# Optimization experiments

Measured on AMD Instinct MI355X. Metric: run time of the kernel, lower is better.

## Reference

```python
import jax, jax.numpy as jnp
import numpy as np

B, T, C = 2, 2048, 2048
H, KVH, HD = 16, 4, 128  # heads, kv heads, head_dim
G = H // KVH             # GQA group size
THETA = 10000.0


def _rope_cos_sin(t, hd, dtype):
    inv_freq = 1.0 / (THETA ** (jnp.arange(0, hd, 2, dtype=jnp.float32) / hd))
    pos = jnp.arange(t, dtype=jnp.float32)
    freqs = pos[:, None] * inv_freq[None, :]          # [T, hd/2]
    emb = jnp.concatenate([freqs, freqs], axis=-1)    # [T, hd]
    return jnp.cos(emb).astype(dtype), jnp.sin(emb).astype(dtype)


def _rotate_half(x):
    x1, x2 = jnp.split(x, 2, axis=-1)
    return jnp.concatenate([-x2, x1], axis=-1)


def setup_inputs() -> dict:
    key = jax.random.key(0)
    ks = jax.random.split(key, 5)
    s_in = 1.0 / np.sqrt(C)
    return {
        "x": jax.random.normal(ks[0], (B, T, C), jnp.float32),
        "wq": jax.random.normal(ks[1], (C, H * HD), jnp.float32) * s_in,
        "bq": jnp.zeros((H * HD,), jnp.float32),
        "wk": jax.random.normal(ks[2], (C, KVH * HD), jnp.float32) * s_in,
        "bk": jnp.zeros((KVH * HD,), jnp.float32),
        "wv": jax.random.normal(ks[3], (C, KVH * HD), jnp.float32) * s_in,
        "bv": jnp.zeros((KVH * HD,), jnp.float32),
        "wo": jax.random.normal(ks[4], (H * HD, C), jnp.float32) * (1.0 / np.sqrt(H * HD)),
    }


def reference(x, wq, bq, wk, bk, wv, bv, wo):
    b, t, c = x.shape
    q = (x @ wq + bq).reshape(b, t, H, HD).transpose(0, 2, 1, 3)    # [B,H,T,hd]
    k = (x @ wk + bk).reshape(b, t, KVH, HD).transpose(0, 2, 1, 3)  # [B,KVH,T,hd]
    v = (x @ wv + bv).reshape(b, t, KVH, HD).transpose(0, 2, 1, 3)

    cos, sin = _rope_cos_sin(t, HD, x.dtype)  # [T,hd]
    q = q * cos + _rotate_half(q) * sin
    k = k * cos + _rotate_half(k) * sin

    # GQA: group query heads over kv heads
    qg = q.reshape(b, KVH, G, t, HD)
    scale = 1.0 / np.sqrt(HD)
    scores = jnp.einsum('bkgtd,bksd->bkgts', qg, k) * scale  # [B,KVH,G,T,T]
    causal = jnp.tril(jnp.ones((t, t), bool))
    scores = jnp.where(causal, scores, jnp.finfo(scores.dtype).min)
    attn = jax.nn.softmax(scores, axis=-1)
    out = jnp.einsum('bkgts,bksd->bkgtd', attn, v)            # [B,KVH,G,T,hd]
    out = out.reshape(b, H, t, HD).transpose(0, 2, 1, 3).reshape(b, t, H * HD)
    return out @ wo
```

## Files before the change

### kernel.cpp

```cpp
#include <hip/hip_runtime.h>
#include <hip/hip_bf16.h>
#include <math.h>

#define B_ 2
#define T_ 2048
#define C_ 2048
#define H_ 16
#define KVH_ 4
#define HD_ 128
#define G_ (H_ / KVH_)
#define MROWS (B_ * T_)
#define NQKV (H_ * HD_ + 2 * KVH_ * HD_)
#define KOFF (H_ * HD_)
#define VOFF (H_ * HD_ + KVH_ * HD_)

typedef __hip_bfloat16 bf16;
typedef short bf16x8 __attribute__((ext_vector_type(8)));
typedef short bf16x4 __attribute__((ext_vector_type(4)));
typedef float f32x4 __attribute__((ext_vector_type(4)));

__device__ __forceinline__ void gload_lds16(const void* g, void* l) {
  __builtin_amdgcn_global_load_lds(
      (const __attribute__((address_space(1))) unsigned int*)g,
      (__attribute__((address_space(3))) unsigned int*)l, 16, 0, 0);
}

static __device__ __forceinline__ f32x4 mfma16(bf16x4 a, bf16x4 b, f32x4 c) {
#if __has_builtin(__builtin_amdgcn_mfma_f32_16x16x16_bf16)
  return __builtin_amdgcn_mfma_f32_16x16x16_bf16(a, b, c, 0, 0, 0);
#else
  return __builtin_amdgcn_mfma_f32_16x16x16bf16_1k(a, b, c, 0, 0, 0);
#endif
}

static __device__ __forceinline__ short f2bf(float x) {
  unsigned u = __builtin_bit_cast(unsigned, x);
  u += 0x7FFFu + ((u >> 16) & 1u);
  return (short)(u >> 16);
}

static __device__ __forceinline__ float fexp2(float x) {
#if __has_builtin(__builtin_amdgcn_exp2f)
  return __builtin_amdgcn_exp2f(x);
#else
  return exp2f(x);
#endif
}

__global__ void cast_bf16_kernel(const float* __restrict__ in, bf16* __restrict__ out, int n) {
  int i = (blockIdx.x * 256 + threadIdx.x) * 4;
  if (i >= n) return;
  float4 v = *(const float4*)(in + i);
  out[i + 0] = __float2bfloat16(v.x);
  out[i + 1] = __float2bfloat16(v.y);
  out[i + 2] = __float2bfloat16(v.z);
  out[i + 3] = __float2bfloat16(v.w);
}

__global__ __launch_bounds__(256) void transpose_cast(const float* __restrict__ in,
                                                      bf16* __restrict__ out,
                                                      int R, int Ccols) {
  __shared__ float t[32][33];
  const int tx = threadIdx.x & 31, ty = threadIdx.x >> 5;
  const int r0 = blockIdx.y * 32, c0 = blockIdx.x * 32;
#pragma unroll
  for (int it = 0; it < 4; ++it)
    t[ty + 8 * it][tx] = in[(size_t)(r0 + ty + 8 * it) * Ccols + c0 + tx];
  __syncthreads();
#pragma unroll
  for (int it = 0; it < 4; ++it)
    out[(size_t)(c0 + ty + 8 * it) * R + r0 + tx] = __float2bfloat16(t[tx][ty + 8 * it]);
}

__global__ __launch_bounds__(256) void transpose_v(const bf16* __restrict__ qkv,
                                                   bf16* __restrict__ vt) {
  __shared__ bf16 t[32][33];
  const int tx = threadIdx.x & 31, ty = threadIdx.x >> 5;
  const int b = blockIdx.z >> 2, kvh = blockIdx.z & 3;
  const int t0 = blockIdx.x * 32, d0 = blockIdx.y * 32;
#pragma unroll
  for (int it = 0; it < 4; ++it)
    t[ty + 8 * it][tx] =
        qkv[(size_t)(b * T_ + t0 + ty + 8 * it) * NQKV + VOFF + kvh * HD_ + d0 + tx];
  __syncthreads();
#pragma unroll
  for (int it = 0; it < 4; ++it)
    vt[((size_t)((b * KVH_ + kvh) * HD_) + d0 + ty + 8 * it) * T_ + t0 + tx] =
        t[tx][ty + 8 * it];
}

__global__ void rope_bf16(bf16* __restrict__ buf, int ld, int col0, int nheads) {
  const int row = blockIdx.x / nheads;
  const int h = blockIdx.x % nheads;
  const int t = row % T_;
  const int d = threadIdx.x;
  bf16* rp = buf + (size_t)row * ld + col0 + h * HD_;
  float vd = __bfloat162float(rp[d]);
  float vp = __bfloat162float(rp[d ^ 64]);
  __syncthreads();
  const int i = d & 63;
  float invf = expf(-(float)(2 * i) * (9.210340371976184f / 128.0f));
  float ang = (float)t * invf;
  float c = cosf(ang), s = sinf(ang);
  rp[d] = __float2bfloat16((d < 64) ? (vd * c - vp * s) : (vd * c + vp * s));
}

template <bool BF16OUT>
__global__ __launch_bounds__(256, 2) void gemm_mfma(
    const bf16* __restrict__ A, const bf16* __restrict__ Bt, void* __restrict__ Cout,
    const float* __restrict__ bq, const float* __restrict__ bk2,
    const float* __restrict__ bv2, int M, int N, int K) {
  __shared__ __align__(16) bf16 As[128 * 32];
  __shared__ __align__(16) bf16 Bs[128 * 32];
  const int tid = threadIdx.x;
  const int w = tid >> 6, lane = tid & 63;
  const int colL = lane & 15, quad = lane >> 4;
  const int wm = w & 1, wn = w >> 1;
  const int r0 = blockIdx.y * 128, c0 = blockIdx.x * 128;

  f32x4 acc[4][4];
  const f32x4 zero = {0.f, 0.f, 0.f, 0.f};
#pragma unroll
  for (int mt = 0; mt < 4; ++mt)
#pragma unroll
    for (int nt = 0; nt < 4; ++nt) acc[mt][nt] = zero;

  for (int k0 = 0; k0 < K; k0 += 32) {
    __syncthreads();
#pragma unroll
    for (int it = 0; it < 2; ++it) {
      const int seg = it * 4 + w;
      const int idx = seg * 64 + lane;
      const int row = idx >> 2, off = idx & 3;
      gload_lds16(A + (size_t)(r0 + row) * K + k0 + off * 8, &As[seg * 512]);
      gload_lds16(Bt + (size_t)(c0 + row) * K + k0 + off * 8, &Bs[seg * 512]);
    }
    __syncthreads();
    bf16x8 af[4], bfv[4];
#pragma unroll
    for (int mt = 0; mt < 4; ++mt)
      af[mt] = *(const bf16x8*)&As[(wm * 64 + mt * 16 + colL) * 32 + quad * 8];
#pragma unroll
    for (int nt = 0; nt < 4; ++nt)
      bfv[nt] = *(const bf16x8*)&Bs[(wn * 64 + nt * 16 + colL) * 32 + quad * 8];
#pragma unroll
    for (int mt = 0; mt < 4; ++mt)
#pragma unroll
      for (int nt = 0; nt < 4; ++nt)
        acc[mt][nt] =
            __builtin_amdgcn_mfma_f32_16x16x32_bf16(af[mt], bfv[nt], acc[mt][nt], 0, 0, 0);
  }

#pragma unroll
  for (int nt = 0; nt < 4; ++nt) {
    const int c = c0 + wn * 64 + nt * 16 + colL;
    float bias = 0.f;
    if (bq) bias = (c < KOFF) ? bq[c] : (c < VOFF ? bk2[c - KOFF] : bv2[c - VOFF]);
#pragma unroll
    for (int mt = 0; mt < 4; ++mt) {
#pragma unroll
      for (int i = 0; i < 4; ++i) {
        const int r = r0 + wm * 64 + mt * 16 + quad * 4 + i;
        const float v = acc[mt][nt][i] + bias;
        if (BF16OUT)
          ((bf16*)Cout)[(size_t)r * N + c] = __float2bfloat16(v);
        else
          ((float*)Cout)[(size_t)r * N + c] = v;
      }
    }
  }
}

#define FA_SCL2 (0.08838834764831845f * 1.4426950408889634f)
#define FA_M2 16.0f

__global__ __launch_bounds__(256, 2) void flash_mfma4(
    const bf16* __restrict__ qkv, const bf16* __restrict__ vt, bf16* __restrict__ ao) {
  __shared__ __align__(16) char smem[32768];
  bf16* Kb0 = (bf16*)smem;
  bf16* Kb1 = (bf16*)(smem + 8192);
  bf16* Vb0 = (bf16*)(smem + 16384);
  bf16* Vb1 = (bf16*)(smem + 24576);

  const int id = blockIdx.x;
  const int hb = id >> 4;
  const int qq = id & 15;
  const int qt = (hb & 1) ? (15 - qq) : qq;
  const int h = hb & 15, b = hb >> 4;
  const int kvh = h >> 2;
  const int q0 = qt * 128;

  const int tid = threadIdx.x;
  const int w = tid >> 6, lane = tid & 63;
  const int colL = lane & 15, quad = lane >> 4;
  const int myq0 = q0 + w * 32;

  const bf16* kg = qkv + (size_t)(b * T_) * NQKV + KOFF + kvh * HD_;
  const bf16* vg = vt + (size_t)((b * KVH_ + kvh) * HD_) * T_;

  auto stageKV = [&](int tile, bf16* kl, bf16* vl) {
    const int s0k = tile * 32;
#pragma unroll
    for (int j = 0; j < 2; ++j) {
      const int s = 2 * w + j;
      const int row = s * 4 + quad;
      const int g = colL ^ (row & 7);
      gload_lds16(kg + (size_t)(s0k + row) * NQKV + g * 8, kl + s * 512);
    }
#pragma unroll
    for (int j = 0; j < 2; ++j) {
      const int s = 2 * w + j;
      const int row = s * 16 + (lane >> 2);
      const int g = (lane & 3) ^ ((row >> 1) & 3);
      gload_lds16(vg + (size_t)row * T_ + s0k + g * 8, vl + s * 512);
    }
  };

  bf16x8 qf[2][4];
  {
    const bf16* qgw = qkv + (size_t)(b * T_ + myq0) * NQKV + h * HD_;
#pragma unroll
    for (int mq = 0; mq < 2; ++mq)
#pragma unroll
      for (int c = 0; c < 4; ++c)
        qf[mq][c] = *(const bf16x8*)(qgw + (size_t)(mq * 16 + colL) * NQKV + c * 32 + quad * 8);
  }

  f32x4 o[2][8];
  const f32x4 zero = {0.f, 0.f, 0.f, 0.f};
#pragma unroll
  for (int mq = 0; mq < 2; ++mq)
#pragma unroll
    for (int ht = 0; ht < 8; ++ht) o[mq][ht] = zero;
  float l_[2] = {0.f, 0.f};

  const int nkv = 4 * qt + 4;
  stageKV(0, Kb0, Vb0);
  asm volatile("s_waitcnt vmcnt(0)\n\ts_barrier" ::: "memory");

  for (int tt = 0; tt < nkv; ++tt) {
    const bf16* Ks = (tt & 1) ? Kb1 : Kb0;
    const bf16* Vs = (tt & 1) ? Vb1 : Vb0;
    if (tt + 1 < nkv) stageKV(tt + 1, (tt & 1) ? Kb0 : Kb1, (tt & 1) ? Vb0 : Vb1);

    const int s0 = tt * 32;
    if (s0 < myq0 + 32) {
      f32x4 s_[2][2];
      s_[0][0] = zero; s_[0][1] = zero; s_[1][0] = zero; s_[1][1] = zero;
#pragma unroll
      for (int c = 0; c < 4; ++c) {
        const int ch = ((c * 4 + quad) ^ (colL & 7)) * 8;
        bf16x8 kf0 = *(const bf16x8*)(Ks + (size_t)colL * 128 + ch);
        bf16x8 kf1 = *(const bf16x8*)(Ks + (size_t)(16 + colL) * 128 + ch);
#pragma unroll
        for (int mq = 0; mq < 2; ++mq) {
          s_[0][mq] = __builtin_amdgcn_mfma_f32_16x16x32_bf16(kf0, qf[mq][c], s_[0][mq], 0, 0, 0);
          s_[1][mq] = __builtin_amdgcn_mfma_f32_16x16x32_bf16(kf1, qf[mq][c], s_[1][mq], 0, 0, 0);
        }
      }

      bf16x4 pf[2][2];
      if (s0 >= myq0) {
#pragma unroll
        for (int kt = 0; kt < 2; ++kt)
#pragma unroll
          for (int mq = 0; mq < 2; ++mq) {
            const int qcol = myq0 + mq * 16 + colL;
            const int kb = s0 + kt * 16 + quad * 4;
            float pv[4];
#pragma unroll
            for (int i = 0; i < 4; ++i) {
              float e = fexp2(fmaf(s_[kt][mq][i], FA_SCL2, -FA_M2));
              pv[i] = (kb + i <= qcol) ? e : 0.f;
            }
            l_[mq] += (pv[0] + pv[1]) + (pv[2] + pv[3]);
            pf[kt][mq] = (bf16x4){f2bf(pv[0]), f2bf(pv[1]), f2bf(pv[2]), f2bf(pv[3])};
          }
      } else {
#pragma unroll
        for (int kt = 0; kt < 2; ++kt)
#pragma unroll
          for (int mq = 0; mq < 2; ++mq) {
            float pv[4];
#pragma unroll
            for (int i = 0; i < 4; ++i)
              pv[i] = fexp2(fmaf(s_[kt][mq][i], FA_SCL2, -FA_M2));
            l_[mq] += (pv[0] + pv[1]) + (pv[2] + pv[3]);
            pf[kt][mq] = (bf16x4){f2bf(pv[0]), f2bf(pv[1]), f2bf(pv[2]), f2bf(pv[3])};
          }
      }

#pragma unroll
      for (int ht = 0; ht < 8; ++ht) {
        const int row = ht * 16 + colL;
#pragma unroll
        for (int kt = 0; kt < 2; ++kt) {
          bf16x4 vf = *(const bf16x4*)(Vs + (size_t)row * 32 +
                                       (((kt * 2 + (quad >> 1)) ^ ((row >> 1) & 3)) * 8) +
                                       (quad & 1) * 4);
#pragma unroll
          for (int mq = 0; mq < 2; ++mq) o[mq][ht] = mfma16(vf, pf[kt][mq], o[mq][ht]);
        }
      }
    }
    asm volatile("s_waitcnt vmcnt(0)\n\ts_barrier" ::: "memory");
  }

#pragma unroll
  for (int mq = 0; mq < 2; ++mq) {
    l_[mq] += __shfl_xor(l_[mq], 16);
    l_[mq] += __shfl_xor(l_[mq], 32);
    const float rl = 1.f / l_[mq];
    const size_t rbase = (size_t)(b * T_ + myq0 + mq * 16 + colL) * (H_ * HD_) + h * HD_;
#pragma unroll
    for (int ht = 0; ht < 8; ++ht) {
      bf16x4 ov;
#pragma unroll
      for (int i = 0; i < 4; ++i) ov[i] = f2bf(o[mq][ht][i] * rl);
      *(bf16x4*)(ao + rbase + ht * 16 + quad * 4) = ov;
    }
  }
}

extern "C" void kernel_launch(void* const* d_in, const int* in_sizes, int n_in,
                              void* d_out, int out_size, void* d_ws, size_t ws_size,
                              hipStream_t stream) {
  (void)in_sizes; (void)n_in; (void)out_size; (void)ws_size;
  const float* x  = (const float*)d_in[0];
  const float* wq = (const float*)d_in[1];
  const float* bq = (const float*)d_in[2];
  const float* wk = (const float*)d_in[3];
  const float* bk = (const float*)d_in[4];
  const float* wv = (const float*)d_in[5];
  const float* bv = (const float*)d_in[6];
  const float* wo = (const float*)d_in[7];
  float* out = (float*)d_out;

  char* ws = (char*)d_ws;
  bf16* xb    = (bf16*)ws;
  bf16* wqkvT = (bf16*)(ws + (16u << 20));
  bf16* woT   = (bf16*)(ws + (28u << 20));
  bf16* qkv   = (bf16*)(ws + (36u << 20));
  bf16* vt    = (bf16*)(ws + (60u << 20));

  cast_bf16_kernel<<<dim3(MROWS * C_ / 1024), dim3(256), 0, stream>>>(x, xb, MROWS * C_);

  transpose_cast<<<dim3(64, 64), dim3(256), 0, stream>>>(wq, wqkvT, C_, 2048);
  transpose_cast<<<dim3(16, 64), dim3(256), 0, stream>>>(wk, wqkvT + (size_t)KOFF * C_, C_, 512);
  transpose_cast<<<dim3(16, 64), dim3(256), 0, stream>>>(wv, wqkvT + (size_t)VOFF * C_, C_, 512);
  transpose_cast<<<dim3(64, 64), dim3(256), 0, stream>>>(wo, woT, 2048, 2048);

  gemm_mfma<true><<<dim3(NQKV / 128, MROWS / 128), dim3(256), 0, stream>>>(
      xb, wqkvT, qkv, bq, bk, bv, MROWS, NQKV, C_);

  rope_bf16<<<dim3(MROWS * H_), dim3(128), 0, stream>>>(qkv, NQKV, 0, H_);
  rope_bf16<<<dim3(MROWS * KVH_), dim3(128), 0, stream>>>(qkv, NQKV, KOFF, KVH_);

  transpose_v<<<dim3(T_ / 32, HD_ / 32, B_ * KVH_), dim3(256), 0, stream>>>(qkv, vt);

  bf16* ao = xb;
  flash_mfma4<<<dim3(512), dim3(256), 0, stream>>>(qkv, vt, ao);

  gemm_mfma<false><<<dim3(C_ / 128, MROWS / 128), dim3(256), 0, stream>>>(
      ao, woT, out, nullptr, nullptr, nullptr, MROWS, C_, KOFF);
}
```

Measured before the change: 358.8 us.

## Halve flash-attention block size, fuse QKV weight transposes, use fast RoPE intrinsics

The flash attention kernel now runs 128-thread blocks (2 waves) covering 64 query rows, with 1024 blocks instead of 512. Tiles are paired as light/heavy in an interleaved order to even out the causal load. Each wave stages twice as many K/V chunks, which cuts the causal tail imbalance but means each K/V tile is reused by fewer query rows. Separately, the three Q/K/V weight transpose launches are merged into one kernel, and RoPE uses exp2 and __sincosf intrinsics instead of expf/cosf/sinf, trading some precision for cheaper math.

```diff
diff --git a/kernel.cpp b/kernel.cpp
--- a/kernel.cpp
+++ b/kernel.cpp
@@ -72,6 +72,27 @@
     out[(size_t)(c0 + ty + 8 * it) * R + r0 + tx] = __float2bfloat16(t[tx][ty + 8 * it]);
 }
 
+__global__ __launch_bounds__(256) void transpose_cast_qkvw(
+    const float* __restrict__ wq, const float* __restrict__ wk,
+    const float* __restrict__ wv, bf16* __restrict__ outT) {
+  __shared__ float t[32][33];
+  const int tx = threadIdx.x & 31, ty = threadIdx.x >> 5;
+  const int r0 = blockIdx.y * 32;
+  const int c0 = blockIdx.x * 32;
+  const float* src;
+  int nn, ld;
+  if (c0 < KOFF)      { src = wq; nn = c0;        ld = 2048; }
+  else if (c0 < VOFF) { src = wk; nn = c0 - KOFF; ld = 512; }
+  else                { src = wv; nn = c0 - VOFF; ld = 512; }
+#pragma unroll
+  for (int it = 0; it < 4; ++it)
+    t[ty + 8 * it][tx] = src[(size_t)(r0 + ty + 8 * it) * ld + nn + tx];
+  __syncthreads();
+#pragma unroll
+  for (int it = 0; it < 4; ++it)
+    outT[(size_t)(c0 + ty + 8 * it) * 2048 + r0 + tx] = __float2bfloat16(t[tx][ty + 8 * it]);
+}
+
 __global__ __launch_bounds__(256) void transpose_v(const bf16* __restrict__ qkv,
                                                    bf16* __restrict__ vt) {
   __shared__ bf16 t[32][33];
@@ -99,9 +120,10 @@
   float vp = __bfloat162float(rp[d ^ 64]);
   __syncthreads();
   const int i = d & 63;
-  float invf = expf(-(float)(2 * i) * (9.210340371976184f / 128.0f));
+  float invf = fexp2(-(float)i * (13.287712379549449f / 64.0f));
   float ang = (float)t * invf;
-  float c = cosf(ang), s = sinf(ang);
+  float s, c;
+  __sincosf(ang, &s, &c);
   rp[d] = __float2bfloat16((d < 64) ? (vd * c - vp * s) : (vd * c + vp * s));
 }
 
@@ -174,7 +196,7 @@
 #define FA_SCL2 (0.08838834764831845f * 1.4426950408889634f)
 #define FA_M2 16.0f
 
-__global__ __launch_bounds__(256, 2) void flash_mfma4(
+__global__ __launch_bounds__(128, 2) void flash_mfma5(
     const bf16* __restrict__ qkv, const bf16* __restrict__ vt, bf16* __restrict__ ao) {
   __shared__ __align__(16) char smem[32768];
   bf16* Kb0 = (bf16*)smem;
@@ -183,17 +205,16 @@
   bf16* Vb1 = (bf16*)(smem + 24576);
 
   const int id = blockIdx.x;
-  const int hb = id >> 4;
-  const int qq = id & 15;
-  const int qt = (hb & 1) ? (15 - qq) : qq;
+  const int hb = id >> 5;
+  const int qq = id & 31;
+  const int qt = (qq & 1) ? (qq >> 1) : (31 - (qq >> 1));
   const int h = hb & 15, b = hb >> 4;
   const int kvh = h >> 2;
-  const int q0 = qt * 128;
 
   const int tid = threadIdx.x;
   const int w = tid >> 6, lane = tid & 63;
   const int colL = lane & 15, quad = lane >> 4;
-  const int myq0 = q0 + w * 32;
+  const int myq0 = qt * 64 + 32 * w;
 
   const bf16* kg = qkv + (size_t)(b * T_) * NQKV + KOFF + kvh * HD_;
   const bf16* vg = vt + (size_t)((b * KVH_ + kvh) * HD_) * T_;
@@ -201,15 +222,15 @@
   auto stageKV = [&](int tile, bf16* kl, bf16* vl) {
     const int s0k = tile * 32;
 #pragma unroll
-    for (int j = 0; j < 2; ++j) {
-      const int s = 2 * w + j;
+    for (int j = 0; j < 4; ++j) {
+      const int s = 4 * w + j;
       const int row = s * 4 + quad;
       const int g = colL ^ (row & 7);
       gload_lds16(kg + (size_t)(s0k + row) * NQKV + g * 8, kl + s * 512);
     }
 #pragma unroll
-    for (int j = 0; j < 2; ++j) {
-      const int s = 2 * w + j;
+    for (int j = 0; j < 4; ++j) {
+      const int s = 4 * w + j;
       const int row = s * 16 + (lane >> 2);
       const int g = (lane & 3) ^ ((row >> 1) & 3);
       gload_lds16(vg + (size_t)row * T_ + s0k + g * 8, vl + s * 512);
@@ -234,7 +255,7 @@
     for (int ht = 0; ht < 8; ++ht) o[mq][ht] = zero;
   float l_[2] = {0.f, 0.f};
 
-  const int nkv = 4 * qt + 4;
+  const int nkv = 2 * qt + 2;
   stageKV(0, Kb0, Vb0);
   asm volatile("s_waitcnt vmcnt(0)\n\ts_barrier" ::: "memory");
 
@@ -345,9 +366,7 @@
 
   cast_bf16_kernel<<<dim3(MROWS * C_ / 1024), dim3(256), 0, stream>>>(x, xb, MROWS * C_);
 
-  transpose_cast<<<dim3(64, 64), dim3(256), 0, stream>>>(wq, wqkvT, C_, 2048);
-  transpose_cast<<<dim3(16, 64), dim3(256), 0, stream>>>(wk, wqkvT + (size_t)KOFF * C_, C_, 512);
-  transpose_cast<<<dim3(16, 64), dim3(256), 0, stream>>>(wv, wqkvT + (size_t)VOFF * C_, C_, 512);
+  transpose_cast_qkvw<<<dim3(96, 64), dim3(256), 0, stream>>>(wq, wk, wv, wqkvT);
   transpose_cast<<<dim3(64, 64), dim3(256), 0, stream>>>(wo, woT, 2048, 2048);
 
   gemm_mfma<true><<<dim3(NQKV / 128, MROWS / 128), dim3(256), 0, stream>>>(
@@ -359,7 +378,7 @@
   transpose_v<<<dim3(T_ / 32, HD_ / 32, B_ * KVH_), dim3(256), 0, stream>>>(qkv, vt);
 
   bf16* ao = xb;
-  flash_mfma4<<<dim3(512), dim3(256), 0, stream>>>(qkv, vt, ao);
+  flash_mfma5<<<dim3(1024), dim3(128), 0, stream>>>(qkv, vt, ao);
 
   gemm_mfma<false><<<dim3(C_ / 128, MROWS / 128), dim3(256), 0, stream>>>(
       ao, woT, out, nullptr, nullptr, nullptr, MROWS, C_, KOFF);
```

After: 354.1 us. Within noise of the previous version (-1.3%).
